# Kernel tuning notes

Hardware: AMD Instinct MI355X
Metric: run time of the kernel (lower is better)

The kernel has to match this reference:

```python
import jax, jax.numpy as jnp
import numpy as np

B, C, T = 256, 1, 16384   # batch, input_channels, seq_len
H = C                      # hidden_size == input_channels in this module
OUT = 1                    # output_channels


def setup_inputs() -> dict:
    key = jax.random.key(0)
    ks = jax.random.split(key, 11)
    # PyTorch GRU/Linear init: uniform(-1/sqrt(H), 1/sqrt(H)); H=1 -> (-1, 1)
    u = lambda k, shape, s=1.0: jax.random.uniform(k, shape, jnp.float32, -s, s)
    s_lin = 1.0 / np.sqrt(2 * H).astype(np.float32)
    return {
        "x": jax.random.normal(ks[0], (B, C, T), jnp.float32),
        # layer 0: input size C, per direction [3H, C] / [3H, H] / [3H]
        "w_ih0": u(ks[1], (2, 3 * H, C)),
        "w_hh0": u(ks[2], (2, 3 * H, H)),
        "b_ih0": u(ks[3], (2, 3 * H)),
        "b_hh0": u(ks[4], (2, 3 * H)),
        # layers 1-2: input size 2H (bidirectional concat)
        "w_ih12": u(ks[5], (2, 2, 3 * H, 2 * H)),
        "w_hh12": u(ks[6], (2, 2, 3 * H, H)),
        "b_ih12": u(ks[7], (2, 2, 3 * H)),
        "b_hh12": u(ks[8], (2, 2, 3 * H)),
        # output projection Linear(2H -> OUT)
        "w_out": u(ks[9], (OUT, 2 * H), s_lin),
        "b_out": u(ks[10], (OUT,), s_lin),
    }


def _gru_dir(xs, w_ih, w_hh, b_ih, b_hh, reverse):
    """One GRU direction. xs: [T, B, in] -> ys: [T, B, H] (time-aligned)."""
    h0 = jnp.zeros((xs.shape[1], w_hh.shape[1]), xs.dtype)

    def step(h, x_t):
        gi = x_t @ w_ih.T + b_ih          # [B, 3H]
        gh = h @ w_hh.T + b_hh            # [B, 3H]
        ir, iz, inn = jnp.split(gi, 3, axis=-1)
        hr, hz, hn = jnp.split(gh, 3, axis=-1)
        r = jax.nn.sigmoid(ir + hr)
        z = jax.nn.sigmoid(iz + hz)
        n = jnp.tanh(inn + r * hn)
        h_new = (1.0 - z) * n + z * h
        return h_new, h_new

    _, ys = jax.lax.scan(step, h0, xs, reverse=reverse)
    return ys


def _bidir(xs, w_ih_f, w_hh_f, b_ih_f, b_hh_f, w_ih_b, w_hh_b, b_ih_b, b_hh_b):
    fwd = _gru_dir(xs, w_ih_f, w_hh_f, b_ih_f, b_hh_f, reverse=False)
    bwd = _gru_dir(xs, w_ih_b, w_hh_b, b_ih_b, b_hh_b, reverse=True)
    return jnp.concatenate([fwd, bwd], axis=-1)  # [T, B, 2H]


def reference(x, w_ih0, w_hh0, b_ih0, b_hh0, w_ih12, w_hh12, b_ih12, b_hh12, w_out, b_out):
    xs = jnp.transpose(x, (2, 0, 1))  # [B, C, T] -> [T, B, C]
    xs = _bidir(xs, w_ih0[0], w_hh0[0], b_ih0[0], b_hh0[0],
                w_ih0[1], w_hh0[1], b_ih0[1], b_hh0[1])
    for l in range(2):  # GRU layers 1 and 2 (structurally distinct weights)
        xs = _bidir(xs, w_ih12[l, 0], w_hh12[l, 0], b_ih12[l, 0], b_hh12[l, 0],
                    w_ih12[l, 1], w_hh12[l, 1], b_ih12[l, 1], b_hh12[l, 1])
    y = xs @ w_out.T + b_out          # [T, B, OUT]
    return jnp.transpose(y, (1, 2, 0))  # [B, OUT, T]
```

## Files before the change

kernel.cpp:

```cpp
#include <hip/hip_runtime.h>
#include <hip/hip_fp16.h>

#define T_LEN 16384
#define B_SZ  256
#define S_CH  256
#define CL    (T_LEN / S_CH)
#define HALO  32
#define SC    16

typedef __attribute__((ext_vector_type(2))) _Float16 h2v;

__device__ __forceinline__ float ex2(float x)  { return __builtin_amdgcn_exp2f(x); }
__device__ __forceinline__ float rcpf(float x) { return __builtin_amdgcn_rcpf(x); }
__device__ __forceinline__ float dot2(h2v a, h2v b, float c)
{ return __builtin_amdgcn_fdot2(a, b, c, false); }

__device__ __forceinline__ float gru_step(float h, float preR, float preZ, float preN,
                                          float UR, float UZ, float UN2, float DN2)
{
    float er  = ex2(fmaf(h, UR, preR));
    float ez  = ex2(fmaf(h, UZ, preZ));
    float r   = rcpf(1.0f + er);
    float z   = rcpf(1.0f + ez);
    float hn2 = fmaf(h, UN2, DN2);
    float en  = ex2(fmaf(r, hn2, preN));
    float n   = fmaf(-2.0f, rcpf(1.0f + en), 1.0f);
    return fmaf(z, h - n, n);
}

template<bool REV>
__device__ __forceinline__ void stageA(const float* __restrict__ x,
        const float* __restrict__ wih, const float* __restrict__ whh,
        const float* __restrict__ bih, const float* __restrict__ bhh,
        __half* __restrict__ l0h, int lane, int b, int a0, int e0)
{
    const int d = REV ? 1 : 0;
    const float L2E = 1.4426950408889634f;
    const float WR  = -L2E * wih[d*3+0];
    const float WZ  = -L2E * wih[d*3+1];
    const float WN  =  2.0f*L2E * wih[d*3+2];
    const float UR  = -L2E * whh[d*3+0];
    const float UZ  = -L2E * whh[d*3+1];
    const float UN2 =  2.0f*L2E * whh[d*3+2];
    const float CR  = -L2E * (bih[d*3+0] + bhh[d*3+0]);
    const float CZ  = -L2E * (bih[d*3+1] + bhh[d*3+1]);
    const float CN  =  2.0f*L2E * bih[d*3+2];
    const float DN2 =  2.0f*L2E * bhh[d*3+2];

    const int warm = REV ? min(HALO, T_LEN - e0) : min(HALO, a0);
    const int nst  = warm + (e0 - a0);
    const int ts   = REV ? (e0 - 1 + warm) : (a0 - warm);
    const float* row = x + (size_t)b * T_LEN;

    float xA[SC], xB[SC];
    float h = 0.0f;

    auto LD = [&](float* F, int base) {
        const float4* p = (const float4*)(row + (REV ? (ts - base - 15) : (ts + base)));
        float4 v0 = p[0], v1 = p[1], v2 = p[2], v3 = p[3];
        float lin[16] = { v0.x,v0.y,v0.z,v0.w, v1.x,v1.y,v1.z,v1.w,
                          v2.x,v2.y,v2.z,v2.w, v3.x,v3.y,v3.z,v3.w };
        #pragma unroll
        for (int k = 0; k < 16; ++k) F[k] = REV ? lin[15 - k] : lin[k];
        __builtin_amdgcn_sched_barrier(0);
    };

    auto CS = [&](float* F, int base) {
        float ov[SC];
        #pragma unroll
        for (int k = 0; k < SC; ++k) {
            float xv = F[k];
            h = gru_step(h, fmaf(xv, WR, CR), fmaf(xv, WZ, CZ), fmaf(xv, WN, CN),
                         UR, UZ, UN2, DN2);
            ov[k] = h;
        }
        if (base >= warm) {
            #pragma unroll
            for (int k = 0; k < SC; ++k) {
                int t = REV ? (ts - (base + k)) : (ts + (base + k));
                l0h[((t - a0) * 64 + lane) * 2 + d] = __float2half_rn(ov[k]);
            }
        }
    };

    LD(xA, 0);
    const int nsup = nst / SC;
    for (int i = 0; i < nsup; i += 2) {
        LD(xB, min((i + 1) * SC, nst - SC));
        CS(xA, i * SC);
        LD(xA, min((i + 2) * SC, nst - SC));
        CS(xB, (i + 1) * SC);
    }
}

template<bool REV>
__device__ __forceinline__ void stageB(const __half* __restrict__ l0h,
        const float* __restrict__ wih, const float* __restrict__ whh,
        const float* __restrict__ bih, const float* __restrict__ bhh,
        __half* __restrict__ l1h, int lane, int a0, int a1, int e1)
{
    const int d = REV ? 1 : 0;
    const float L2E = 1.4426950408889634f;
    const h2v WRp = { (_Float16)(-L2E * wih[(d*3+0)*2+0]),
                      (_Float16)(-L2E * wih[(d*3+0)*2+1]) };
    const h2v WZp = { (_Float16)(-L2E * wih[(d*3+1)*2+0]),
                      (_Float16)(-L2E * wih[(d*3+1)*2+1]) };
    const h2v WNp = { (_Float16)(2.0f*L2E * wih[(d*3+2)*2+0]),
                      (_Float16)(2.0f*L2E * wih[(d*3+2)*2+1]) };
    const float UR  = -L2E * whh[d*3+0];
    const float UZ  = -L2E * whh[d*3+1];
    const float UN2 =  2.0f*L2E * whh[d*3+2];
    const float CR  = -L2E * (bih[d*3+0] + bhh[d*3+0]);
    const float CZ  = -L2E * (bih[d*3+1] + bhh[d*3+1]);
    const float CN  =  2.0f*L2E * bih[d*3+2];
    const float DN2 =  2.0f*L2E * bhh[d*3+2];

    const int warm = REV ? min(HALO, T_LEN - e1) : min(HALO, a1);
    const int nst  = warm + (e1 - a1);
    const int ts   = REV ? (e1 - 1 + warm) : (a1 - warm);
    const h2v* src = (const h2v*)l0h;

    h2v vA[SC], vB[SC];
    float h = 0.0f;

#define LDB(V, base_) { int base = (base_); \
    _Pragma("unroll") for (int k = 0; k < SC; ++k) { \
      int t = REV ? (ts - (base + k)) : (ts + (base + k)); \
      V[k] = src[(t - a0) * 64 + lane]; } \
    __builtin_amdgcn_sched_barrier(0); }

#define CSB12(V, base_) { int base = (base_); float ov[SC]; \
    _Pragma("unroll") for (int k = 0; k < SC; ++k) { \
      float pr = dot2(V[k], WRp, CR); \
      float pz = dot2(V[k], WZp, CZ); \
      float pn = dot2(V[k], WNp, CN); \
      h = gru_step(h, pr, pz, pn, UR, UZ, UN2, DN2); ov[k] = h; } \
    if (base >= warm) { \
      _Pragma("unroll") for (int k = 0; k < SC; ++k) { \
        int t = REV ? (ts - (base + k)) : (ts + (base + k)); \
        l1h[((t - a1) * 64 + lane) * 2 + d] = __float2half_rn(ov[k]); } } }

    LDB(vA, 0);
    const int nsup = nst / SC;
    for (int i = 0; i < nsup; i += 2) {
        LDB(vB, min((i + 1) * SC, nst - SC));
        CSB12(vA, i * SC);
        LDB(vA, min((i + 2) * SC, nst - SC));
        CSB12(vB, (i + 1) * SC);
    }
#undef LDB
#undef CSB12
}

__global__ void __launch_bounds__(128) k_all(const float* __restrict__ x,
        const float* __restrict__ w_ih0, const float* __restrict__ w_hh0,
        const float* __restrict__ b_ih0, const float* __restrict__ b_hh0,
        const float* __restrict__ w_ih12, const float* __restrict__ w_hh12,
        const float* __restrict__ b_ih12, const float* __restrict__ b_hh12,
        const float* __restrict__ wo, const float* __restrict__ bo,
        float* __restrict__ y)
{
    __shared__ __align__(16) char smem[81920];
    __half* l0h = (__half*)smem;
    __half* l1h = (__half*)(smem + 49152);
    float (*tY)[65] = (float(*)[65])smem;

    const int blk  = blockIdx.x;
    const int xcd  = blk & 7;
    const int jj   = blk >> 3;
    const int sl   = jj & 31;
    const int bg   = jj >> 5;
    const int s    = xcd * 32 + sl;
    const int lane = threadIdx.x & 63;
    const int w    = threadIdx.x >> 6;
    const int b    = bg * 64 + lane;
    const int sg   = w ? -1 : 1;
    const int t0   = s * CL;

    const int WCf = min(HALO, t0);
    const int WCb = min(HALO, T_LEN - (t0 + CL));
    const int a1  = t0 - WCf, e1 = t0 + CL + WCb;
    const int WBf = min(HALO, a1);
    const int WBb = min(HALO, T_LEN - e1);
    const int a0  = a1 - WBf, e0 = e1 + WBb;

    if (w == 0) stageA<false>(x, w_ih0, w_hh0, b_ih0, b_hh0, l0h, lane, b, a0, e0);
    else        stageA<true >(x, w_ih0, w_hh0, b_ih0, b_hh0, l0h, lane, b, a0, e0);
    __syncthreads();

    if (w == 0) stageB<false>(l0h, w_ih12, w_hh12, b_ih12, b_hh12, l1h, lane, a0, a1, e1);
    else        stageB<true >(l0h, w_ih12, w_hh12, b_ih12, b_hh12, l1h, lane, a0, a1, e1);
    __syncthreads();

    {
        const float* wih = w_ih12 + 12;
        const float* whh = w_hh12 + 6;
        const float* bih = b_ih12 + 6;
        const float* bhh = b_hh12 + 6;
        const int d = w;
        const float L2E = 1.4426950408889634f;
        const h2v WRp = { (_Float16)(-L2E * wih[(d*3+0)*2+0]),
                          (_Float16)(-L2E * wih[(d*3+0)*2+1]) };
        const h2v WZp = { (_Float16)(-L2E * wih[(d*3+1)*2+0]),
                          (_Float16)(-L2E * wih[(d*3+1)*2+1]) };
        const h2v WNp = { (_Float16)(2.0f*L2E * wih[(d*3+2)*2+0]),
                          (_Float16)(2.0f*L2E * wih[(d*3+2)*2+1]) };
        const float UR  = -L2E * whh[d*3+0];
        const float UZ  = -L2E * whh[d*3+1];
        const float UN2 =  2.0f*L2E * whh[d*3+2];
        const float CR  = -L2E * (bih[d*3+0] + bhh[d*3+0]);
        const float CZ  = -L2E * (bih[d*3+1] + bhh[d*3+1]);
        const float CN  =  2.0f*L2E * bih[d*3+2];
        const float DN2 =  2.0f*L2E * bhh[d*3+2];

        const int warm   = w ? WCb : WCf;
        const int tstart = w ? (e1 - 1) : a1;
        const h2v* src = (const h2v*)l1h;

        h2v vA[SC], vB[SC];
        float f[CL];
        float h = 0.0f;

#define LD2(V, base_) { int base = (base_); \
    _Pragma("unroll") for (int k = 0; k < SC; ++k) { \
      int t = tstart + sg * (base + k); \
      V[k] = src[(t - a1) * 64 + lane]; } \
    __builtin_amdgcn_sched_barrier(0); }

#define CSB(V) { \
    _Pragma("unroll") for (int k = 0; k < SC; ++k) { \
      float pr = dot2(V[k], WRp, CR); \
      float pz = dot2(V[k], WZp, CZ); \
      float pn = dot2(V[k], WNp, CN); \
      h = gru_step(h, pr, pz, pn, UR, UZ, UN2, DN2); } }

#define CSS(V, Q) { \
    _Pragma("unroll") for (int k = 0; k < SC; ++k) { \
      float pr = dot2(V[k], WRp, CR); \
      float pz = dot2(V[k], WZp, CZ); \
      float pn = dot2(V[k], WNp, CN); \
      h = gru_step(h, pr, pz, pn, UR, UZ, UN2, DN2); \
      f[(Q) * SC + k] = h; } }

        LD2(vA, 0);
        if (warm) {
            LD2(vB, SC);      CSB(vA);
            LD2(vA, 2 * SC);  CSB(vB);
        }
        LD2(vB, warm + SC);      CSS(vA, 0);
        LD2(vA, warm + 2 * SC);  CSS(vB, 1);
        LD2(vB, warm + 3 * SC);  CSS(vA, 2);
                                 CSS(vB, 3);
#undef LD2
#undef CSB
#undef CSS

        const float wf = wo[0], wb = wo[1], bias = bo[0];
        if (w == 0) {
            #pragma unroll
            for (int m = 0; m < CL; ++m) tY[lane][m] = fmaf(wf, f[m], bias);
        }
        __syncthreads();
        if (w == 1) {
            #pragma unroll
            for (int m = 0; m < CL; ++m) tY[lane][CL - 1 - m] += wb * f[m];
        }
        __syncthreads();
        {
            const int b0 = bg * 64;
            const int c4 = threadIdx.x & 15;
            const int r  = (threadIdx.x >> 4) & 7;
            #pragma unroll
            for (int i = 0; i < 8; ++i) {
                int brow = r + 8 * i;
                float4 v = make_float4(tY[brow][c4*4+0], tY[brow][c4*4+1],
                                       tY[brow][c4*4+2], tY[brow][c4*4+3]);
                ((float4*)y)[(size_t)(b0 + brow) * (T_LEN / 4) + (t0 >> 2) + c4] = v;
            }
        }
    }
}

extern "C" void kernel_launch(void* const* d_in, const int* in_sizes, int n_in,
                              void* d_out, int out_size, void* d_ws, size_t ws_size,
                              hipStream_t stream)
{
    (void)in_sizes; (void)n_in; (void)out_size; (void)d_ws; (void)ws_size;
    const float* x      = (const float*)d_in[0];
    const float* w_ih0  = (const float*)d_in[1];
    const float* w_hh0  = (const float*)d_in[2];
    const float* b_ih0  = (const float*)d_in[3];
    const float* b_hh0  = (const float*)d_in[4];
    const float* w_ih12 = (const float*)d_in[5];
    const float* w_hh12 = (const float*)d_in[6];
    const float* b_ih12 = (const float*)d_in[7];
    const float* b_hh12 = (const float*)d_in[8];
    const float* w_out  = (const float*)d_in[9];
    const float* b_out  = (const float*)d_in[10];
    float* y = (float*)d_out;

    k_all<<<4 * S_CH, 128, 0, stream>>>(x, w_ih0, w_hh0, b_ih0, b_hh0,
                                        w_ih12, w_hh12, b_ih12, b_hh12,
                                        w_out, b_out, y);
}
```

Measured before the change: 144.8 us.

## Move layer-0 intermediates to global scratch to shrink LDS and raise occupancy

Stores the layer-0 GRU outputs in a per-block global workspace, as separate forward and backward fp16 planes, instead of in shared memory. This cuts the LDS footprint from 80KB to 32KB and adds a min-blocks hint of 2 to launch bounds, so more blocks can be resident per CU. Layer 1 now reads each timestep with two scalar fp16 global loads instead of one packed LDS read, and an extra barrier guards reuse of the LDS tile. The trade is higher-latency global/L2 traffic and a dependence on workspace size (1024 blocks times 48KB) in exchange for better latency hiding on this latency-bound serial recurrence.

```diff
diff --git a/kernel.cpp b/kernel.cpp
--- a/kernel.cpp
+++ b/kernel.cpp
@@ -7,6 +7,8 @@
 #define CL    (T_LEN / S_CH)
 #define HALO  32
 #define SC    16
+#define L0PLN 12288
+#define SCRB  49152
 
 typedef __attribute__((ext_vector_type(2))) _Float16 h2v;
 
@@ -32,7 +34,7 @@
 __device__ __forceinline__ void stageA(const float* __restrict__ x,
         const float* __restrict__ wih, const float* __restrict__ whh,
         const float* __restrict__ bih, const float* __restrict__ bhh,
-        __half* __restrict__ l0h, int lane, int b, int a0, int e0)
+        _Float16* __restrict__ l0p, int lane, int b, int a0, int e0)
 {
     const int d = REV ? 1 : 0;
     const float L2E = 1.4426950408889634f;
@@ -78,7 +80,7 @@
             #pragma unroll
             for (int k = 0; k < SC; ++k) {
                 int t = REV ? (ts - (base + k)) : (ts + (base + k));
-                l0h[((t - a0) * 64 + lane) * 2 + d] = __float2half_rn(ov[k]);
+                l0p[(t - a0) * 64 + lane] = (_Float16)ov[k];
             }
         }
     };
@@ -94,7 +96,8 @@
 }
 
 template<bool REV>
-__device__ __forceinline__ void stageB(const __half* __restrict__ l0h,
+__device__ __forceinline__ void stageB(
+        const _Float16* __restrict__ l0f, const _Float16* __restrict__ l0b,
         const float* __restrict__ wih, const float* __restrict__ whh,
         const float* __restrict__ bih, const float* __restrict__ bhh,
         __half* __restrict__ l1h, int lane, int a0, int a1, int e1)
@@ -118,15 +121,15 @@
     const int warm = REV ? min(HALO, T_LEN - e1) : min(HALO, a1);
     const int nst  = warm + (e1 - a1);
     const int ts   = REV ? (e1 - 1 + warm) : (a1 - warm);
-    const h2v* src = (const h2v*)l0h;
 
     h2v vA[SC], vB[SC];
     float h = 0.0f;
 
 #define LDB(V, base_) { int base = (base_); \
     _Pragma("unroll") for (int k = 0; k < SC; ++k) { \
-      int t = REV ? (ts - (base + k)) : (ts + (base + k)); \
-      V[k] = src[(t - a0) * 64 + lane]; } \
+      int t   = REV ? (ts - (base + k)) : (ts + (base + k)); \
+      int idx = (t - a0) * 64 + lane; \
+      V[k] = (h2v){ l0f[idx], l0b[idx] }; } \
     __builtin_amdgcn_sched_barrier(0); }
 
 #define CSB12(V, base_) { int base = (base_); float ov[SC]; \
@@ -152,17 +155,16 @@
 #undef CSB12
 }
 
-__global__ void __launch_bounds__(128) k_all(const float* __restrict__ x,
+__global__ void __launch_bounds__(128, 2) k_all(const float* __restrict__ x,
         const float* __restrict__ w_ih0, const float* __restrict__ w_hh0,
         const float* __restrict__ b_ih0, const float* __restrict__ b_hh0,
         const float* __restrict__ w_ih12, const float* __restrict__ w_hh12,
         const float* __restrict__ b_ih12, const float* __restrict__ b_hh12,
         const float* __restrict__ wo, const float* __restrict__ bo,
-        float* __restrict__ y)
-{
-    __shared__ __align__(16) char smem[81920];
-    __half* l0h = (__half*)smem;
-    __half* l1h = (__half*)(smem + 49152);
+        char* __restrict__ ws, float* __restrict__ y)
+{
+    __shared__ __align__(16) char smem[32768];
+    __half* l1h = (__half*)smem;
     float (*tY)[65] = (float(*)[65])smem;
 
     const int blk  = blockIdx.x;
@@ -177,6 +179,9 @@
     const int sg   = w ? -1 : 1;
     const int t0   = s * CL;
 
+    _Float16* l0f = (_Float16*)(ws + (size_t)blk * SCRB);
+    _Float16* l0b = l0f + L0PLN;
+
     const int WCf = min(HALO, t0);
     const int WCb = min(HALO, T_LEN - (t0 + CL));
     const int a1  = t0 - WCf, e1 = t0 + CL + WCb;
@@ -184,12 +189,12 @@
     const int WBb = min(HALO, T_LEN - e1);
     const int a0  = a1 - WBf, e0 = e1 + WBb;
 
-    if (w == 0) stageA<false>(x, w_ih0, w_hh0, b_ih0, b_hh0, l0h, lane, b, a0, e0);
-    else        stageA<true >(x, w_ih0, w_hh0, b_ih0, b_hh0, l0h, lane, b, a0, e0);
+    if (w == 0) stageA<false>(x, w_ih0, w_hh0, b_ih0, b_hh0, l0f, lane, b, a0, e0);
+    else        stageA<true >(x, w_ih0, w_hh0, b_ih0, b_hh0, l0b, lane, b, a0, e0);
     __syncthreads();
 
-    if (w == 0) stageB<false>(l0h, w_ih12, w_hh12, b_ih12, b_hh12, l1h, lane, a0, a1, e1);
-    else        stageB<true >(l0h, w_ih12, w_hh12, b_ih12, b_hh12, l1h, lane, a0, a1, e1);
+    if (w == 0) stageB<false>(l0f, l0b, w_ih12, w_hh12, b_ih12, b_hh12, l1h, lane, a0, a1, e1);
+    else        stageB<true >(l0f, l0b, w_ih12, w_hh12, b_ih12, b_hh12, l1h, lane, a0, a1, e1);
     __syncthreads();
 
     {
@@ -255,6 +260,7 @@
 #undef CSB
 #undef CSS
 
+        __syncthreads();
         const float wf = wo[0], wb = wo[1], bias = bo[0];
         if (w == 0) {
             #pragma unroll
@@ -285,7 +291,7 @@
                               void* d_out, int out_size, void* d_ws, size_t ws_size,
                               hipStream_t stream)
 {
-    (void)in_sizes; (void)n_in; (void)out_size; (void)d_ws; (void)ws_size;
+    (void)in_sizes; (void)n_in; (void)out_size; (void)ws_size;
     const float* x      = (const float*)d_in[0];
     const float* w_ih0  = (const float*)d_in[1];
     const float* w_hh0  = (const float*)d_in[2];
@@ -301,5 +307,5 @@
 
     k_all<<<4 * S_CH, 128, 0, stream>>>(x, w_ih0, w_hh0, b_ih0, b_hh0,
                                         w_ih12, w_hh12, b_ih12, b_hh12,
-                                        w_out, b_out, y);
-}
+                                        w_out, b_out, (char*)d_ws, y);
+}
```

Measured after the change: 146.6 us. About the same (+1.2%).
